# Kernel optimization log

Hardware: AMD Instinct MI355X
Metric: run time of the kernel (lower is better)

Reference implementation:

```python
import jax, jax.numpy as jnp
import numpy as np

N, IN, H, C = 50000, 128, 256, 64
E_G, E_K = 600000, 800000
MLP_H = H // 2  # multiplier=2 (residual=False)
EPS = 1e-5


def _w(k, i, o):
    return (jax.random.normal(k, (i, o), jnp.float32) * np.float32(1.0 / np.sqrt(i)))


def setup_inputs() -> dict:
    key = jax.random.key(0)
    ks = jax.random.split(key, 32)
    inp = {
        "feat": jax.random.normal(ks[0], (N, IN), jnp.float32),
        "g_src": jax.random.randint(ks[1], (E_G,), 0, N, jnp.int32),
        "g_dst": jax.random.randint(ks[2], (E_G,), 0, N, jnp.int32),
        "k_src": jax.random.randint(ks[3], (E_K,), 0, N, jnp.int32),
        "k_dst": jax.random.randint(ks[4], (E_K,), 0, N, jnp.int32),
        # local GraphSAGE: 3 SAGEConv layers (IN->H, H->H, H->H)
        "lw_self_0": _w(ks[5], IN, H), "lw_neigh_0": _w(ks[6], IN, H), "lb_0": jnp.zeros((H,), jnp.float32),
        "lw_self_1": _w(ks[7], H, H),  "lw_neigh_1": _w(ks[8], H, H),  "lb_1": jnp.zeros((H,), jnp.float32),
        "lw_self_2": _w(ks[9], H, H),  "lw_neigh_2": _w(ks[10], H, H), "lb_2": jnp.zeros((H,), jnp.float32),
        # global GraphSAGE: 2 SAGEConv layers (IN->H, H->H)
        "gw_self_0": _w(ks[11], IN, H), "gw_neigh_0": _w(ks[12], IN, H), "gb_0": jnp.zeros((H,), jnp.float32),
        "gw_self_1": _w(ks[13], H, H),  "gw_neigh_1": _w(ks[14], H, H),  "gb_1": jnp.zeros((H,), jnp.float32),
        # MLP head: Linear(2H -> MLP_H), BatchNorm1d(MLP_H), ReLU, Linear(MLP_H -> C)
        "mlp_w1": _w(ks[15], 2 * H, MLP_H), "mlp_b1": jnp.zeros((MLP_H,), jnp.float32),
        "bn_gamma": jnp.ones((MLP_H,), jnp.float32), "bn_beta": jnp.zeros((MLP_H,), jnp.float32),
        "mlp_w2": _w(ks[16], MLP_H, C), "mlp_b2": jnp.zeros((C,), jnp.float32),
    }
    return inp


def sage_conv(src, dst, h, w_self, w_neigh, b):
    # DGL SAGEConv, mean aggregator: fc_self(h) + fc_neigh(mean_{u in N(v)} h_u) + bias
    msg = h[src]                                             # [E, d] irregular gather
    agg = jax.ops.segment_sum(msg, dst, num_segments=N)      # [N, d] irregular scatter-add
    deg = jax.ops.segment_sum(jnp.ones(src.shape, h.dtype), dst, num_segments=N)
    h_neigh = agg / jnp.maximum(deg, 1.0)[:, None]           # isolated nodes -> 0
    return h @ w_self + h_neigh @ w_neigh + b


def batch_norm(x, gamma, beta):
    mu = jnp.mean(x, axis=0)
    var = jnp.mean(jnp.square(x - mu), axis=0)  # biased var, as in torch BN forward
    return gamma * (x - mu) * jax.lax.rsqrt(var + EPS) + beta


def reference(feat, g_src, g_dst, k_src, k_dst,
              lw_self_0, lw_neigh_0, lb_0, lw_self_1, lw_neigh_1, lb_1,
              lw_self_2, lw_neigh_2, lb_2,
              gw_self_0, gw_neigh_0, gb_0, gw_self_1, gw_neigh_1, gb_1,
              mlp_w1, mlp_b1, bn_gamma, bn_beta, mlp_w2, mlp_b2):
    # local GraphSAGE (3 layers, relu between; dropout = identity in eval)
    h = feat
    h = jax.nn.relu(sage_conv(g_src, g_dst, h, lw_self_0, lw_neigh_0, lb_0))
    h = jax.nn.relu(sage_conv(g_src, g_dst, h, lw_self_1, lw_neigh_1, lb_1))
    local_emb = sage_conv(g_src, g_dst, h, lw_self_2, lw_neigh_2, lb_2)
    # global GraphSAGE on knn graph (2 layers)
    h = feat
    h = jax.nn.relu(sage_conv(k_src, k_dst, h, gw_self_0, gw_neigh_0, gb_0))
    global_emb = sage_conv(k_src, k_dst, h, gw_self_1, gw_neigh_1, gb_1)
    # fuse + BatchNorm-MLP head
    x = jnp.concatenate([local_emb, global_emb], axis=1)     # [N, 2H]
    x = x @ mlp_w1 + mlp_b1
    x = jax.nn.relu(batch_norm(x, bn_gamma, bn_beta))
    return x @ mlp_w2 + mlp_b2                               # [N, C]
```

## Files before the change

### kernel.cpp

```cpp
#include <hip/hip_runtime.h>

#define NN   50000
#define IN_F 128
#define HF   256
#define COUT 64
#define MLPH 128
#define EG   600000
#define EK   800000
#define RNG  6250
#define CAPG 80000
#define CAPK 106000
#define BN_EPS 1e-5f

typedef __attribute__((ext_vector_type(8))) short short8;
typedef __attribute__((ext_vector_type(8))) unsigned short ushort8;
typedef __attribute__((ext_vector_type(4))) float f32x4;

__device__ __forceinline__ unsigned short f2bf(float f) {
  union { float f; unsigned int u; } v; v.f = f;
  unsigned int r = v.u + 0x7FFFu + ((v.u >> 16) & 1u);
  return (unsigned short)(r >> 16);
}
__device__ __forceinline__ float bf2f(unsigned short s) {
  union { unsigned int u; float f; } v; v.u = ((unsigned int)s) << 16;
  return v.f;
}

__device__ __forceinline__ void gload_lds16(const void* g, void* l) {
  __builtin_amdgcn_global_load_lds((const __attribute__((address_space(1))) void*)g,
                                   (__attribute__((address_space(3))) void*)l, 16, 0, 0);
}

struct WDesc { const float* src; int rows; int cshift; int kofs; int ldk; int dofs; };
struct WPack { WDesc d[12]; };

__global__ __launch_bounds__(256) void prep_kernel(const float* __restrict__ feat,
                                                   unsigned short* __restrict__ featbf,
                                                   WPack p, unsigned short* __restrict__ wts) {
  int b = blockIdx.x;
  if (b < 3126) {
    int i = b * 256 + threadIdx.x;
    if (i < NN * IN_F / 8) {
      float4 a = *reinterpret_cast<const float4*>(&feat[i * 8]);
      float4 c = *reinterpret_cast<const float4*>(&feat[i * 8 + 4]);
      ushort8 o;
      o[0] = f2bf(a.x); o[1] = f2bf(a.y); o[2] = f2bf(a.z); o[3] = f2bf(a.w);
      o[4] = f2bf(c.x); o[5] = f2bf(c.y); o[6] = f2bf(c.z); o[7] = f2bf(c.w);
      *reinterpret_cast<ushort8*>(&featbf[i * 8]) = o;
    }
  } else {
    int wb = b - 3126;
    WDesc w = p.d[wb >> 5];
    int xb = wb & 31;
    int total = w.rows << w.cshift;
    int cmask = (1 << w.cshift) - 1;
    for (int idx = xb * 256 + threadIdx.x; idx < total; idx += 32 * 256) {
      int r = idx >> w.cshift, c = idx & cmask;
      wts[w.dofs + (size_t)c * w.ldk + w.kofs + r] = f2bf(w.src[idx]);
    }
  }
}

__global__ __launch_bounds__(128) void fuse_w_kernel(
    const float* __restrict__ wl2s, const float* __restrict__ wl2n,
    const float* __restrict__ wg1s, const float* __restrict__ wg1n,
    const float* __restrict__ w1, const float* __restrict__ bl2,
    const float* __restrict__ bg1, const float* __restrict__ b1,
    unsigned short* __restrict__ wf, float* __restrict__ bfused) {
  int b = blockIdx.x;
  int c = threadIdx.x;
  __shared__ float row[256];
  if (b < 1024) {
    int seg = b >> 8, i = b & 255;
    const float* W = (seg == 0) ? wl2s : (seg == 1) ? wl2n : (seg == 2) ? wg1s : wg1n;
    const float* w1b = w1 + ((seg < 2) ? 0 : 256) * MLPH;
    row[c] = W[i * 256 + c];
    row[c + 128] = W[i * 256 + 128 + c];
    __syncthreads();
    float acc = 0.f;
    for (int o = 0; o < 256; ++o) acc += row[o] * w1b[o * MLPH + c];
    unsigned short v = f2bf(acc);
    if (seg == 0)      wf[(size_t)c * 512 + i] = v;
    else if (seg == 2) wf[(size_t)c * 512 + 256 + i] = v;
    else if (seg == 1) wf[65536 + (size_t)c * 256 + i] = v;
    else               wf[98304 + (size_t)c * 256 + i] = v;
  } else {
    float acc = b1[c];
    for (int o = 0; o < 256; ++o) acc += bl2[o] * w1[o * MLPH + c];
    for (int o = 0; o < 256; ++o) acc += bg1[o] * w1[(256 + o) * MLPH + c];
    bfused[c] = acc;
  }
}

__global__ __launch_bounds__(256) void bucket_kernel(const int* __restrict__ g_src,
                                                     const int* __restrict__ g_dst,
                                                     const int* __restrict__ k_src,
                                                     const int* __restrict__ k_dst,
                                                     int* __restrict__ gcnt,
                                                     unsigned* __restrict__ bkt_g,
                                                     unsigned* __restrict__ bkt_k) {
  __shared__ unsigned buf[2048];
  __shared__ int rcnt[8], rbase[8], roff[8];
  const int gr = blockIdx.y;
  const int* src = gr ? k_src : g_src;
  const int* dst = gr ? k_dst : g_dst;
  unsigned* bkt = gr ? bkt_k : bkt_g;
  const int CAP = gr ? CAPK : CAPG;
  const int E = gr ? EK : EG;
  int* gc = gcnt + gr * 8;
  const int tid = threadIdx.x;
  const int e0 = blockIdx.x * 2048;
  if (e0 >= E) return;
  if (tid < 8) rcnt[tid] = 0;
  __syncthreads();
  unsigned vloc[8];
  int rloc[8], ploc[8];
#pragma unroll
  for (int i = 0; i < 8; ++i) {
    int e = e0 + i * 256 + tid;
    rloc[i] = -1;
    if (e < E) {
      int d = dst[e], s = src[e];
      int r = d / RNG;
      vloc[i] = ((unsigned)d << 16) | (unsigned)s;
      rloc[i] = r;
      ploc[i] = atomicAdd(&rcnt[r], 1);
    }
  }
  __syncthreads();
  if (tid == 0) {
    int acc = 0;
#pragma unroll
    for (int r = 0; r < 8; ++r) { roff[r] = acc; acc += rcnt[r]; }
  }
  __syncthreads();
#pragma unroll
  for (int i = 0; i < 8; ++i)
    if (rloc[i] >= 0) buf[roff[rloc[i]] + ploc[i]] = vloc[i];
  __syncthreads();
  if (tid < 8) rbase[tid] = atomicAdd(&gc[tid], rcnt[tid]);
  __syncthreads();
#pragma unroll
  for (int r = 0; r < 8; ++r) {
    int len = rcnt[r];
    unsigned* dstp = bkt + (size_t)r * CAP + rbase[r];
    for (int i = tid; i < len; i += 256) dstp[i] = buf[roff[r] + i];
  }
}

__global__ __launch_bounds__(256) void count_bucket(const unsigned* __restrict__ bkt_g,
                                                    const unsigned* __restrict__ bkt_k,
                                                    const int* __restrict__ gcnt,
                                                    int* __restrict__ cnt_g,
                                                    int* __restrict__ cnt_k, int CC) {
  __shared__ int hist[RNG];
  const int r = blockIdx.x, gr = blockIdx.y, z = blockIdx.z;
  const unsigned* b = (gr ? bkt_k : bkt_g) + (size_t)r * (gr ? CAPK : CAPG);
  int* cnt = gr ? cnt_k : cnt_g;
  const int n = gcnt[gr * 8 + r];
  const unsigned lo = r * RNG;
  for (int i = threadIdx.x; i < RNG; i += 256) hist[i] = 0;
  __syncthreads();
  for (int i = z * 256 + threadIdx.x; i < n; i += CC * 256) {
    unsigned d = (b[i] >> 16) - lo;
    atomicAdd(&hist[d], 1);
  }
  __syncthreads();
  for (int i = threadIdx.x; i < RNG; i += 256) {
    int v = hist[i];
    if (v) atomicAdd(&cnt[lo + i], v);
  }
}

__global__ __launch_bounds__(256) void scan_partial2(const int* __restrict__ cnt_g,
                                                     const int* __restrict__ cnt_k,
                                                     int* __restrict__ part, int n) {
  const int* cnt = blockIdx.y ? cnt_k : cnt_g;
  int* pp = part + blockIdx.y * 256;
  int i = blockIdx.x * 256 + threadIdx.x;
  int v = (i < n) ? cnt[i] : 0;
  __shared__ int ws[4];
  int lane = threadIdx.x & 63, wid = threadIdx.x >> 6;
  int x = v;
#pragma unroll
  for (int d = 1; d < 64; d <<= 1) { int y = __shfl_up(x, d, 64); if (lane >= d) x += y; }
  if (lane == 63) ws[wid] = x;
  __syncthreads();
  if (threadIdx.x == 0) pp[blockIdx.x] = ws[0] + ws[1] + ws[2] + ws[3];
}

__global__ __launch_bounds__(256) void scan_block2(int* __restrict__ part, int np) {
  int* pp = part + blockIdx.x * 256;
  __shared__ int ws[4];
  int tid = threadIdx.x, lane = tid & 63, wid = tid >> 6;
  int v = (tid < np) ? pp[tid] : 0;
  int x = v;
#pragma unroll
  for (int d = 1; d < 64; d <<= 1) { int y = __shfl_up(x, d, 64); if (lane >= d) x += y; }
  if (lane == 63) ws[wid] = x;
  __syncthreads();
  int add = 0;
#pragma unroll
  for (int k = 0; k < 4; ++k) if (k < wid) add += ws[k];
  if (tid < np) pp[tid] = x - v + add;
}

__global__ __launch_bounds__(256) void scan_final2(const int* __restrict__ cnt_g,
                                                   const int* __restrict__ cnt_k,
                                                   const int* __restrict__ part,
                                                   int* __restrict__ off_g,
                                                   int* __restrict__ off_k,
                                                   float* __restrict__ invg,
                                                   float* __restrict__ invk, int n) {
  const int* cnt = blockIdx.y ? cnt_k : cnt_g;
  const int* pp = part + blockIdx.y * 256;
  int* off = blockIdx.y ? off_k : off_g;
  float* inv = blockIdx.y ? invk : invg;
  int total = blockIdx.y ? EK : EG;
  int i = blockIdx.x * 256 + threadIdx.x;
  int v = (i < n) ? cnt[i] : 0;
  __shared__ int ws[4];
  int lane = threadIdx.x & 63, wid = threadIdx.x >> 6;
  int x = v;
#pragma unroll
  for (int d = 1; d < 64; d <<= 1) { int y = __shfl_up(x, d, 64); if (lane >= d) x += y; }
  if (lane == 63) ws[wid] = x;
  __syncthreads();
  int add = pp[blockIdx.x];
#pragma unroll
  for (int k = 0; k < 4; ++k) if (k < wid) add += ws[k];
  if (i < n) {
    off[i] = x - v + add;
    inv[i] = 1.0f / fmaxf((float)v, 1.0f);
  }
  if (i == 0) off[n] = total;
}

__global__ __launch_bounds__(256) void fill_bucket(const unsigned* __restrict__ bkt_g,
                                                   const unsigned* __restrict__ bkt_k,
                                                   const int* __restrict__ gcnt,
                                                   const int* __restrict__ off_g,
                                                   const int* __restrict__ off_k,
                                                   int* __restrict__ cur_g,
                                                   int* __restrict__ cur_k,
                                                   unsigned short* __restrict__ e16g,
                                                   unsigned short* __restrict__ e16k, int FC) {
  const int r = blockIdx.x, gr = blockIdx.y, z = blockIdx.z;
  const unsigned* b = (gr ? bkt_k : bkt_g) + (size_t)r * (gr ? CAPK : CAPG);
  const int* off = gr ? off_k : off_g;
  int* cur = gr ? cur_k : cur_g;
  unsigned short* e16 = gr ? e16k : e16g;
  const int n = gcnt[gr * 8 + r];
  for (int i = z * 256 + (int)threadIdx.x; i < n; i += FC * 256) {
    unsigned v = b[i];
    int d = v >> 16;
    int pz = atomicAdd(&cur[d], 1);
    e16[off[d] + pz] = (unsigned short)(v & 0xffffu);
  }
}

template <int DLOG2>
__global__ __launch_bounds__(256) void csr_aggregate(const unsigned short* __restrict__ h,
                                                     const int* __restrict__ off,
                                                     const unsigned short* __restrict__ esrc,
                                                     const float* __restrict__ inv,
                                                     unsigned short* __restrict__ out) {
  constexpr int TPN = (1 << DLOG2) / 8;
  constexpr int NPB = 256 / TPN;
  int node = blockIdx.x * NPB + ((int)threadIdx.x / TPN);
  int lane = threadIdx.x & (TPN - 1);
  if (node >= NN) return;
  int s = off[node], e = off[node + 1];
  float acc[8] = {0.f, 0.f, 0.f, 0.f, 0.f, 0.f, 0.f, 0.f};
  int j = s;
  for (; j + 3 < e; j += 4) {
    int s0 = esrc[j], s1 = esrc[j + 1], s2 = esrc[j + 2], s3 = esrc[j + 3];
    ushort8 v0 = *reinterpret_cast<const ushort8*>(&h[((size_t)s0 << DLOG2) + lane * 8]);
    ushort8 v1 = *reinterpret_cast<const ushort8*>(&h[((size_t)s1 << DLOG2) + lane * 8]);
    ushort8 v2 = *reinterpret_cast<const ushort8*>(&h[((size_t)s2 << DLOG2) + lane * 8]);
    ushort8 v3 = *reinterpret_cast<const ushort8*>(&h[((size_t)s3 << DLOG2) + lane * 8]);
#pragma unroll
    for (int i = 0; i < 8; ++i) acc[i] += bf2f(v0[i]);
#pragma unroll
    for (int i = 0; i < 8; ++i) acc[i] += bf2f(v1[i]);
#pragma unroll
    for (int i = 0; i < 8; ++i) acc[i] += bf2f(v2[i]);
#pragma unroll
    for (int i = 0; i < 8; ++i) acc[i] += bf2f(v3[i]);
  }
  for (; j < e; ++j) {
    int s0 = esrc[j];
    ushort8 v0 = *reinterpret_cast<const ushort8*>(&h[((size_t)s0 << DLOG2) + lane * 8]);
#pragma unroll
    for (int i = 0; i < 8; ++i) acc[i] += bf2f(v0[i]);
  }
  float sc = inv[node];
  ushort8 o;
#pragma unroll
  for (int i = 0; i < 8; ++i) o[i] = f2bf(acc[i] * sc);
  *reinterpret_cast<ushort8*>(&out[((size_t)node << DLOG2) + lane * 8]) = o;
}

template <int K1, int K2, bool RELU, bool OUT_BF16>
__global__ __launch_bounds__(256) void gemm_gl(
    const unsigned short* __restrict__ A1, const unsigned short* __restrict__ A2,
    const unsigned short* __restrict__ Bt, const float* __restrict__ bias,
    void* __restrict__ outv, int ldo, int nrows) {
  constexpr int KTOT = K1 + K2;
  constexpr int KT = KTOT / 64;
  __shared__ char smem[32768];
  unsigned short* sA = (unsigned short*)smem;
  unsigned short* sB = sA + 8192;

  const int t = threadIdx.x;
  const int lane = t & 63;
  const int w = t >> 6;
  const int wm = (w & 1) * 64, wn = (w >> 1) * 64;
  const int row0 = blockIdx.y * 128;
  const int n0 = blockIdx.x * 128;

  const int srow = (w << 5) + (lane >> 3);
  const int schunk = (lane & 7) << 3;

  f32x4 acc[4][4] = {};

  for (int kt = 0; kt < KT; ++kt) {
    const int kbase = kt * 64;
    const unsigned short* Asrc = (kbase < K1) ? A1 : A2;
    const int kA = (kbase < K1) ? kbase : (kbase - K1);
    const int lda = (kbase < K1) ? K1 : K2;
#pragma unroll
    for (int q = 0; q < 4; ++q) {
      int rA = srow + q * 8;
      int rowg = row0 + rA;
      if (rowg >= nrows) rowg = nrows - 1;
      gload_lds16(Asrc + (size_t)rowg * lda + kA + schunk,
                  sA + ((w << 5) + q * 8) * 64);
      gload_lds16(Bt + (size_t)(n0 + rA) * KTOT + kbase + schunk,
                  sB + ((w << 5) + q * 8) * 64);
    }
    __syncthreads();
#pragma unroll
    for (int kk = 0; kk < 2; ++kk) {
      const int ko = kk * 32 + (lane >> 4) * 8;
      short8 a[4], b[4];
#pragma unroll
      for (int mi = 0; mi < 4; ++mi)
        a[mi] = *reinterpret_cast<const short8*>(&sA[(wm + mi * 16 + (lane & 15)) * 64 + ko]);
#pragma unroll
      for (int ni = 0; ni < 4; ++ni)
        b[ni] = *reinterpret_cast<const short8*>(&sB[(wn + ni * 16 + (lane & 15)) * 64 + ko]);
#pragma unroll
      for (int mi = 0; mi < 4; ++mi)
#pragma unroll
        for (int ni = 0; ni < 4; ++ni)
          acc[mi][ni] = __builtin_amdgcn_mfma_f32_16x16x32_bf16(a[mi], b[ni], acc[mi][ni], 0, 0, 0);
    }
    __syncthreads();
  }

  float* Co = (float*)smem;
#pragma unroll
  for (int h = 0; h < 2; ++h) {
    __syncthreads();
    if ((w >> 1) == h) {
#pragma unroll
      for (int mi = 0; mi < 4; ++mi)
#pragma unroll
        for (int ni = 0; ni < 4; ++ni) {
          int col = ni * 16 + (lane & 15);
          int rowb = wm + mi * 16 + (lane >> 4) * 4;
#pragma unroll
          for (int j = 0; j < 4; ++j) Co[(rowb + j) * 64 + col] = acc[mi][ni][j];
        }
    }
    __syncthreads();
    int sr = t >> 1, cb = (t & 1) * 32;
    int r = row0 + sr;
    if (r < nrows) {
      float v[32];
#pragma unroll
      for (int i = 0; i < 32; ++i) {
        v[i] = Co[sr * 64 + cb + i] + bias[n0 + h * 64 + cb + i];
        if (RELU) v[i] = fmaxf(v[i], 0.f);
      }
      if (OUT_BF16) {
        unsigned short* dst = (unsigned short*)outv + (size_t)r * ldo + n0 + h * 64 + cb;
#pragma unroll
        for (int q = 0; q < 4; ++q) {
          ushort8 o;
#pragma unroll
          for (int i = 0; i < 8; ++i) o[i] = f2bf(v[q * 8 + i]);
          *reinterpret_cast<ushort8*>(dst + q * 8) = o;
        }
      } else {
        float* dst = (float*)outv + (size_t)r * ldo + n0 + h * 64 + cb;
#pragma unroll
        for (int q = 0; q < 8; ++q) {
          float4 o = make_float4(v[4 * q], v[4 * q + 1], v[4 * q + 2], v[4 * q + 3]);
          *reinterpret_cast<float4*>(dst + 4 * q) = o;
        }
      }
    }
  }
}

__global__ __launch_bounds__(256) void gemm_tail512(
    const unsigned short* __restrict__ A0, const unsigned short* __restrict__ A1,
    const unsigned short* __restrict__ Bt, const float* __restrict__ bias,
    const unsigned short* __restrict__ aYL, const unsigned short* __restrict__ aYG,
    float* __restrict__ outv, int nrows) {
  constexpr int KTOT = 512;
  constexpr int KT = 8;
  __shared__ char smem[32768];
  unsigned short* sA = (unsigned short*)smem;
  unsigned short* sB = sA + 8192;

  const int t = threadIdx.x;
  const int lane = t & 63;
  const int w = t >> 6;
  const int wm = (w & 1) * 64, wn = (w >> 1) * 64;
  const int row0 = blockIdx.y * 128;

  const int srow = (w << 5) + (lane >> 3);
  const int schunk = (lane & 7) << 3;

  f32x4 acc[4][4] = {};

  for (int kt = 0; kt < KT; ++kt) {
    const unsigned short* Asrc = (kt < 4) ? A0 : A1;
    const int kA = (kt & 3) * 64;
#pragma unroll
    for (int q = 0; q < 4; ++q) {
      int rA = srow + q * 8;
      int rowg = row0 + rA;
      if (rowg >= nrows) rowg = nrows - 1;
      gload_lds16(Asrc + (size_t)rowg * 256 + kA + schunk,
                  sA + ((w << 5) + q * 8) * 64);
      gload_lds16(Bt + (size_t)rA * KTOT + kt * 64 + schunk,
                  sB + ((w << 5) + q * 8) * 64);
    }
    __syncthreads();
#pragma unroll
    for (int kk = 0; kk < 2; ++kk) {
      const int ko = kk * 32 + (lane >> 4) * 8;
      short8 a[4], b[4];
#pragma unroll
      for (int mi = 0; mi < 4; ++mi)
        a[mi] = *reinterpret_cast<const short8*>(&sA[(wm + mi * 16 + (lane & 15)) * 64 + ko]);
#pragma unroll
      for (int ni = 0; ni < 4; ++ni)
        b[ni] = *reinterpret_cast<const short8*>(&sB[(wn + ni * 16 + (lane & 15)) * 64 + ko]);
#pragma unroll
      for (int mi = 0; mi < 4; ++mi)
#pragma unroll
        for (int ni = 0; ni < 4; ++ni)
          acc[mi][ni] = __builtin_amdgcn_mfma_f32_16x16x32_bf16(a[mi], b[ni], acc[mi][ni], 0, 0, 0);
    }
    __syncthreads();
  }

  float* Co = (float*)smem;
#pragma unroll
  for (int h = 0; h < 2; ++h) {
    __syncthreads();
    if ((w >> 1) == h) {
#pragma unroll
      for (int mi = 0; mi < 4; ++mi)
#pragma unroll
        for (int ni = 0; ni < 4; ++ni) {
          int col = ni * 16 + (lane & 15);
          int rowb = wm + mi * 16 + (lane >> 4) * 4;
#pragma unroll
          for (int j = 0; j < 4; ++j) Co[(rowb + j) * 64 + col] = acc[mi][ni][j];
        }
    }
    __syncthreads();
    int sr = t >> 1, cb = (t & 1) * 32;
    int r = row0 + sr;
    if (r < nrows) {
      float* dst = outv + (size_t)r * MLPH + h * 64 + cb;
#pragma unroll
      for (int q = 0; q < 4; ++q) {
        ushort8 ya = *reinterpret_cast<const ushort8*>(&aYL[(size_t)r * MLPH + h * 64 + cb + q * 8]);
        ushort8 yb = *reinterpret_cast<const ushort8*>(&aYG[(size_t)r * MLPH + h * 64 + cb + q * 8]);
        float v[8];
#pragma unroll
        for (int i = 0; i < 8; ++i)
          v[i] = Co[sr * 64 + cb + q * 8 + i] + bf2f(ya[i]) + bf2f(yb[i]) +
                 bias[h * 64 + cb + q * 8 + i];
        *reinterpret_cast<float4*>(dst + q * 8) = make_float4(v[0], v[1], v[2], v[3]);
        *reinterpret_cast<float4*>(dst + q * 8 + 4) = make_float4(v[4], v[5], v[6], v[7]);
      }
    }
  }
}

__global__ __launch_bounds__(256) void bn_stats_kernel(const float* __restrict__ x,
                                                       float* __restrict__ sums,
                                                       float* __restrict__ sumsq) {
  int c = threadIdx.x & 127;
  int rbase = (blockIdx.x * 256 + threadIdx.x) >> 7;
  int stride = (gridDim.x * 256) >> 7;
  float s = 0.f, s2 = 0.f;
  for (int r = rbase; r < NN; r += stride) {
    float v = x[(size_t)r * 128 + c];
    s += v;
    s2 += v * v;
  }
  __shared__ float ls[256], ls2[256];
  ls[threadIdx.x] = s;
  ls2[threadIdx.x] = s2;
  __syncthreads();
  if (threadIdx.x < 128) {
    s = ls[threadIdx.x] + ls[threadIdx.x + 128];
    s2 = ls2[threadIdx.x] + ls2[threadIdx.x + 128];
    atomicAdd(&sums[c], s);
    atomicAdd(&sumsq[c], s2);
  }
}

__global__ __launch_bounds__(128) void bn_finalize_kernel(float* __restrict__ stats,
                                                          const float* __restrict__ gamma,
                                                          const float* __restrict__ beta) {
  int c = threadIdx.x;
  float mu = stats[c] * (1.0f / NN);
  float var = stats[128 + c] * (1.0f / NN) - mu * mu;
  var = fmaxf(var, 0.f);
  float sc = gamma[c] * rsqrtf(var + BN_EPS);
  stats[256 + c] = sc;
  stats[384 + c] = beta[c] - mu * sc;
}

template <int K1, bool RELU>
__global__ __launch_bounds__(256) void gemm_mfma_bn(
    const float* __restrict__ A1v, const unsigned short* __restrict__ Bt,
    const float* __restrict__ bias, const float* __restrict__ bnscale,
    const float* __restrict__ bnshift, float* __restrict__ outv, int ldo, int nrows) {
  constexpr int KT = K1 / 64;
  constexpr int LDT = 72;
  __shared__ char smem[2 * 64 * LDT * 2];
  unsigned short* As = (unsigned short*)smem;
  unsigned short* Bs = As + 64 * LDT;
  float* Co = (float*)smem;
  constexpr int LDC = 68;

  const int t = threadIdx.x;
  const int lane = t & 63;
  const int w = t >> 6;
  const int wm = (w & 1) * 32, wn = (w >> 1) * 32;
  const int row0 = blockIdx.y * 64;
  const int n0 = blockIdx.x * 64;

  const int sr = t >> 2;
  const int skc = (t & 3) * 16;
  int rg = row0 + sr;
  if (rg >= nrows) rg = nrows - 1;

  f32x4 acc[2][2] = {};

  for (int kt = 0; kt < KT; ++kt) {
    const int kbase = kt * 64;
    {
      const float* xb = A1v + (size_t)rg * K1 + kbase + skc;
      ushort8 o0, o1;
#pragma unroll
      for (int i = 0; i < 8; ++i) {
        float v = xb[i] * bnscale[kbase + skc + i] + bnshift[kbase + skc + i];
        o0[i] = f2bf(fmaxf(v, 0.f));
      }
#pragma unroll
      for (int i = 0; i < 8; ++i) {
        float v = xb[8 + i] * bnscale[kbase + skc + 8 + i] + bnshift[kbase + skc + 8 + i];
        o1[i] = f2bf(fmaxf(v, 0.f));
      }
      *reinterpret_cast<ushort8*>(&As[sr * LDT + skc]) = o0;
      *reinterpret_cast<ushort8*>(&As[sr * LDT + skc + 8]) = o1;
    }
    {
      const unsigned short* bb = Bt + (size_t)(n0 + sr) * K1 + kbase + skc;
      int4 p0 = *reinterpret_cast<const int4*>(bb);
      int4 p1 = *reinterpret_cast<const int4*>(bb + 8);
      *reinterpret_cast<int4*>(&Bs[sr * LDT + skc]) = p0;
      *reinterpret_cast<int4*>(&Bs[sr * LDT + skc + 8]) = p1;
    }
    __syncthreads();
#pragma unroll
    for (int kk = 0; kk < 2; ++kk) {
      const int ko = kk * 32 + (lane >> 4) * 8;
      short8 a0 = *reinterpret_cast<const short8*>(&As[(wm + (lane & 15)) * LDT + ko]);
      short8 a1 = *reinterpret_cast<const short8*>(&As[(wm + 16 + (lane & 15)) * LDT + ko]);
      short8 b0 = *reinterpret_cast<const short8*>(&Bs[(wn + (lane & 15)) * LDT + ko]);
      short8 b1 = *reinterpret_cast<const short8*>(&Bs[(wn + 16 + (lane & 15)) * LDT + ko]);
      acc[0][0] = __builtin_amdgcn_mfma_f32_16x16x32_bf16(a0, b0, acc[0][0], 0, 0, 0);
      acc[0][1] = __builtin_amdgcn_mfma_f32_16x16x32_bf16(a0, b1, acc[0][1], 0, 0, 0);
      acc[1][0] = __builtin_amdgcn_mfma_f32_16x16x32_bf16(a1, b0, acc[1][0], 0, 0, 0);
      acc[1][1] = __builtin_amdgcn_mfma_f32_16x16x32_bf16(a1, b1, acc[1][1], 0, 0, 0);
    }
    __syncthreads();
  }

#pragma unroll
  for (int mi = 0; mi < 2; ++mi)
#pragma unroll
    for (int ni = 0; ni < 2; ++ni) {
      int col = wn + ni * 16 + (lane & 15);
      int rowb = wm + mi * 16 + (lane >> 4) * 4;
#pragma unroll
      for (int j = 0; j < 4; ++j) Co[(rowb + j) * LDC + col] = acc[mi][ni][j];
    }
  __syncthreads();
  {
    int r = row0 + sr;
    if (r < nrows) {
      float v[16];
#pragma unroll
      for (int i = 0; i < 16; ++i) {
        v[i] = Co[sr * LDC + skc + i] + bias[n0 + skc + i];
        if (RELU) v[i] = fmaxf(v[i], 0.f);
      }
      float* dst = outv + (size_t)r * ldo + n0 + skc;
#pragma unroll
      for (int i = 0; i < 4; ++i) {
        float4 o = make_float4(v[4 * i], v[4 * i + 1], v[4 * i + 2], v[4 * i + 3]);
        *reinterpret_cast<float4*>(dst + 4 * i) = o;
      }
    }
  }
}

extern "C" void kernel_launch(void* const* d_in, const int* in_sizes, int n_in,
                              void* d_out, int out_size, void* d_ws, size_t ws_size,
                              hipStream_t stream) {
  const float* feat = (const float*)d_in[0];
  const int* g_src = (const int*)d_in[1];
  const int* g_dst = (const int*)d_in[2];
  const int* k_src = (const int*)d_in[3];
  const int* k_dst = (const int*)d_in[4];
  const float* lb_0 = (const float*)d_in[7];
  const float* lb_1 = (const float*)d_in[10];
  const float* lb_2 = (const float*)d_in[13];
  const float* gb_0 = (const float*)d_in[16];
  const float* gb_1 = (const float*)d_in[19];
  const float* mlp_b1 = (const float*)d_in[21];
  const float* bn_gamma = (const float*)d_in[22];
  const float* bn_beta = (const float*)d_in[23];
  const float* mlp_b2 = (const float*)d_in[25];
  float* out = (float*)d_out;

  float* xf32 = (float*)d_ws;
  int* cnt_g = (int*)(xf32 + (size_t)NN * 128);
  int* cnt_k = cnt_g + NN;
  int* cur_g = cnt_k + NN;
  int* cur_k = cur_g + NN;
  float* stats = (float*)(cur_k + NN);
  int* gcnt = (int*)(stats + 512);
  float* zbias = (float*)(gcnt + 16);
  float* invg = zbias + 128;
  float* invk = invg + NN;
  int* off_g = (int*)(invk + NN);
  int* off_k = off_g + NN + 4;
  int* part = off_k + NN + 4;
  unsigned* bkt_g = (unsigned*)(part + 512);
  unsigned* bkt_k = bkt_g + 8 * CAPG;
  unsigned short* e16g = (unsigned short*)(bkt_k + 8 * CAPK);
  unsigned short* e16k = e16g + EG;
  unsigned short* featbf = e16k + EK;
  unsigned short* wts = featbf + (size_t)NN * IN_F;
  unsigned short* wf = wts + 598016;
  float* bfused = (float*)(wf + 131072);
  unsigned short* bfA = (unsigned short*)(bfused + 128);
  unsigned short* bfB = bfA + (size_t)NN * HF;
  unsigned short* bfAgg = bfB + (size_t)NN * HF;
  unsigned short* bfYL = bfAgg + (size_t)NN * HF;
  unsigned short* bfYG = bfYL + (size_t)NN * MLPH;
  unsigned short* bfAYL = bfYG + (size_t)NN * MLPH;
  unsigned short* bfAYG = bfAYL + (size_t)NN * MLPH;

  const int wL0 = 0, wL1 = 65536, wG0 = 327680, wH2 = 589824;
  const int wfYL = 65536, wfYG = 98304;

  dim3 blk(256);
  const int NB = (NN + 255) / 256;
  const int MB = (NN + 127) / 128;
  const dim3 gridH(2, MB);
  const dim3 gridM(1, MB);
  const int agg128_blocks = (NN + 15) / 16;
  const int agg256_blocks = (NN + 7) / 8;
  const int BKB = (EK + 2047) / 2048;
  const int CC = 8;
  const int FC = 16;

  hipMemsetAsync(cnt_g, 0,
                 (size_t)(4 * NN) * sizeof(int) + 512 * sizeof(float) + 16 * sizeof(int) +
                     128 * sizeof(float),
                 stream);

  WPack p;
  p.d[0] = {(const float*)d_in[5], 128, 8, 0, 256, wL0};
  p.d[1] = {(const float*)d_in[6], 128, 8, 128, 256, wL0};
  p.d[2] = {(const float*)d_in[8], 256, 8, 0, 512, wL1};
  p.d[3] = {(const float*)d_in[9], 256, 8, 256, 512, wL1};
  p.d[4] = {(const float*)d_in[11], 256, 8, 0, 512, 196608};
  p.d[5] = {(const float*)d_in[12], 256, 8, 256, 512, 196608};
  p.d[6] = {(const float*)d_in[14], 128, 8, 0, 256, wG0};
  p.d[7] = {(const float*)d_in[15], 128, 8, 128, 256, wG0};
  p.d[8] = {(const float*)d_in[17], 256, 8, 0, 512, 393216};
  p.d[9] = {(const float*)d_in[18], 256, 8, 256, 512, 393216};
  p.d[10] = {(const float*)d_in[20], 512, 7, 0, 512, 524288};
  p.d[11] = {(const float*)d_in[24], 128, 6, 0, 128, wH2};
  prep_kernel<<<3510, blk, 0, stream>>>(feat, featbf, p, wts);

  fuse_w_kernel<<<1025, 128, 0, stream>>>(
      (const float*)d_in[11], (const float*)d_in[12],
      (const float*)d_in[17], (const float*)d_in[18],
      (const float*)d_in[20], lb_2, gb_1, mlp_b1, wf, bfused);

  bucket_kernel<<<dim3(BKB, 2), blk, 0, stream>>>(g_src, g_dst, k_src, k_dst, gcnt, bkt_g, bkt_k);
  count_bucket<<<dim3(8, 2, CC), blk, 0, stream>>>(bkt_g, bkt_k, gcnt, cnt_g, cnt_k, CC);
  scan_partial2<<<dim3(NB, 2), blk, 0, stream>>>(cnt_g, cnt_k, part, NN);
  scan_block2<<<2, blk, 0, stream>>>(part, NB);
  scan_final2<<<dim3(NB, 2), blk, 0, stream>>>(cnt_g, cnt_k, part, off_g, off_k, invg, invk, NN);
  fill_bucket<<<dim3(8, 2, FC), blk, 0, stream>>>(bkt_g, bkt_k, gcnt, off_g, off_k,
                                                  cur_g, cur_k, e16g, e16k, FC);

  csr_aggregate<7><<<agg128_blocks, blk, 0, stream>>>(featbf, off_g, e16g, invg, bfAgg);
  gemm_gl<128, 128, true, true><<<gridH, blk, 0, stream>>>(
      featbf, bfAgg, wts + wL0, lb_0, bfA, HF, NN);
  csr_aggregate<8><<<agg256_blocks, blk, 0, stream>>>(bfA, off_g, e16g, invg, bfAgg);
  gemm_gl<256, 256, true, true><<<gridH, blk, 0, stream>>>(
      bfA, bfAgg, wts + wL1, lb_1, bfB, HF, NN);
  gemm_gl<256, 0, false, true><<<gridM, blk, 0, stream>>>(
      bfB, nullptr, wf + wfYL, zbias, bfYL, MLPH, NN);
  csr_aggregate<7><<<agg128_blocks, blk, 0, stream>>>(bfYL, off_g, e16g, invg, bfAYL);
  csr_aggregate<7><<<agg128_blocks, blk, 0, stream>>>(featbf, off_k, e16k, invk, bfAgg);
  gemm_gl<128, 128, true, true><<<gridH, blk, 0, stream>>>(
      featbf, bfAgg, wts + wG0, gb_0, bfA, HF, NN);
  gemm_gl<256, 0, false, true><<<gridM, blk, 0, stream>>>(
      bfA, nullptr, wf + wfYG, zbias, bfYG, MLPH, NN);
  csr_aggregate<7><<<agg128_blocks, blk, 0, stream>>>(bfYG, off_k, e16k, invk, bfAYG);

  gemm_tail512<<<gridM, blk, 0, stream>>>(bfB, bfA, wf, bfused, bfAYL, bfAYG, xf32, NN);

  bn_stats_kernel<<<256, blk, 0, stream>>>(xf32, stats, stats + 128);
  bn_finalize_kernel<<<1, 128, 0, stream>>>(stats, bn_gamma, bn_beta);

  gemm_mfma_bn<128, false><<<dim3(1, (NN + 63) / 64), blk, 0, stream>>>(
      xf32, wts + wH2, mlp_b2, stats + 256, stats + 384, out, COUT, NN);
}
```

Before: 506.8 us.

## Fill CSR edge lists with LDS cursor atomics per destination sub-range

Replaces the global-atomic fill kernel with one that splits each destination bucket into four sub-ranges. Each 1024-thread block keeps the write cursors for its sub-range in shared memory, seeded from the CSR offsets. Every block scans its whole bucket and keeps only the edges in its sub-range. This turns global atomics into LDS atomics and drops the cur arrays along with their memset. In exchange, each bucket is read four times and only 64 blocks run, so the GPU may be underused.

New measurement: 486.8 us. -3.9%, faster.

```diff
diff --git a/kernel.cpp b/kernel.cpp
--- a/kernel.cpp
+++ b/kernel.cpp
@@ -8,6 +8,7 @@
 #define EG   600000
 #define EK   800000
 #define RNG  6250
+#define SUBR 1563
 #define CAPG 80000
 #define CAPK 106000
 #define BN_EPS 1e-5f
@@ -236,26 +237,34 @@
   if (i == 0) off[n] = total;
 }
 
-__global__ __launch_bounds__(256) void fill_bucket(const unsigned* __restrict__ bkt_g,
-                                                   const unsigned* __restrict__ bkt_k,
-                                                   const int* __restrict__ gcnt,
-                                                   const int* __restrict__ off_g,
-                                                   const int* __restrict__ off_k,
-                                                   int* __restrict__ cur_g,
-                                                   int* __restrict__ cur_k,
-                                                   unsigned short* __restrict__ e16g,
-                                                   unsigned short* __restrict__ e16k, int FC) {
-  const int r = blockIdx.x, gr = blockIdx.y, z = blockIdx.z;
-  const unsigned* b = (gr ? bkt_k : bkt_g) + (size_t)r * (gr ? CAPK : CAPG);
+__global__ __launch_bounds__(1024) void fill_sub(const unsigned* __restrict__ bkt_g,
+                                                 const unsigned* __restrict__ bkt_k,
+                                                 const int* __restrict__ gcnt,
+                                                 const int* __restrict__ off_g,
+                                                 const int* __restrict__ off_k,
+                                                 unsigned short* __restrict__ e16g,
+                                                 unsigned short* __restrict__ e16k) {
+  __shared__ int curs[SUBR];
+  const int b = blockIdx.x;
+  const int s = b & 3, r = (b >> 2) & 7, gr = b >> 5;
+  const unsigned* bkt = (gr ? bkt_k : bkt_g) + (size_t)r * (gr ? CAPK : CAPG);
   const int* off = gr ? off_k : off_g;
-  int* cur = gr ? cur_k : cur_g;
   unsigned short* e16 = gr ? e16k : e16g;
   const int n = gcnt[gr * 8 + r];
-  for (int i = z * 256 + (int)threadIdx.x; i < n; i += FC * 256) {
-    unsigned v = b[i];
-    int d = v >> 16;
-    int pz = atomicAdd(&cur[d], 1);
-    e16[off[d] + pz] = (unsigned short)(v & 0xffffu);
+  const int lo = r * RNG;
+  const int slo = s * SUBR;
+  int send = slo + SUBR;
+  if (send > RNG) send = RNG;
+  const int swid = send - slo;
+  for (int i = threadIdx.x; i < swid; i += 1024) curs[i] = off[lo + slo + i];
+  __syncthreads();
+  for (int i = threadIdx.x; i < n; i += 1024) {
+    unsigned v = bkt[i];
+    int d = (int)(v >> 16) - lo - slo;
+    if ((unsigned)d < (unsigned)swid) {
+      int pz = atomicAdd(&curs[d], 1);
+      e16[pz] = (unsigned short)(v & 0xffffu);
+    }
   }
 }
 
@@ -651,9 +660,7 @@
   float* xf32 = (float*)d_ws;
   int* cnt_g = (int*)(xf32 + (size_t)NN * 128);
   int* cnt_k = cnt_g + NN;
-  int* cur_g = cnt_k + NN;
-  int* cur_k = cur_g + NN;
-  float* stats = (float*)(cur_k + NN);
+  float* stats = (float*)(cnt_k + NN);
   int* gcnt = (int*)(stats + 512);
   float* zbias = (float*)(gcnt + 16);
   float* invg = zbias + 128;
@@ -689,10 +696,9 @@
   const int agg256_blocks = (NN + 7) / 8;
   const int BKB = (EK + 2047) / 2048;
   const int CC = 8;
-  const int FC = 16;
 
   hipMemsetAsync(cnt_g, 0,
-                 (size_t)(4 * NN) * sizeof(int) + 512 * sizeof(float) + 16 * sizeof(int) +
+                 (size_t)(2 * NN) * sizeof(int) + 512 * sizeof(float) + 16 * sizeof(int) +
                      128 * sizeof(float),
                  stream);
 
@@ -721,8 +727,7 @@
   scan_partial2<<<dim3(NB, 2), blk, 0, stream>>>(cnt_g, cnt_k, part, NN);
   scan_block2<<<2, blk, 0, stream>>>(part, NB);
   scan_final2<<<dim3(NB, 2), blk, 0, stream>>>(cnt_g, cnt_k, part, off_g, off_k, invg, invk, NN);
-  fill_bucket<<<dim3(8, 2, FC), blk, 0, stream>>>(bkt_g, bkt_k, gcnt, off_g, off_k,
-                                                  cur_g, cur_k, e16g, e16k, FC);
+  fill_sub<<<64, 1024, 0, stream>>>(bkt_g, bkt_k, gcnt, off_g, off_k, e16g, e16k);
 
   csr_aggregate<7><<<agg128_blocks, blk, 0, stream>>>(featbf, off_g, e16g, invg, bfAgg);
   gemm_gl<128, 128, true, true><<<gridH, blk, 0, stream>>>(
```
